# Optimization experiments

Hardware: AMD Instinct MI355X
Metric: run time of the kernel (lower is better)

Reference implementation:

```python
import jax, jax.numpy as jnp
import numpy as np

LOG2PI = float(np.log(2.0 * np.pi))
EPS_SHIFT = -0.5   # self.eps
TAU = 0.5          # self.tau
ETA = 1.0          # self.eta
MAG_A = 5500.0     # magnitude remap constants from forward()
MAG_B = 1100.0


def setup_inputs() -> dict:
    key = jax.random.key(0)
    k1, k2, k3, k4, k5 = jax.random.split(key, 5)
    B, K, C = 4096, 128, 64
    z = jax.random.normal(k1, (B, K, 2), dtype=jnp.float32)
    # per-keypoint mixture weights summing to 1 (GMM weights_)
    weights = jax.nn.softmax(jax.random.normal(k2, (K, C), dtype=jnp.float32), axis=-1)
    means = jax.random.normal(k3, (K, C, 2), dtype=jnp.float32)
    # SPD covariances: A A^T + 0.2 I
    A = jax.random.normal(k4, (K, C, 2, 2), dtype=jnp.float32) * 0.3
    covs = jnp.einsum('kcij,kclj->kcil', A, A) + 0.2 * jnp.eye(2, dtype=jnp.float32)
    # latent_stats unnormalization factor per latent coordinate (2/(max-min))
    scale = jax.random.uniform(k5, (K, 2), dtype=jnp.float32, minval=0.5, maxval=2.0)
    return {"z": z, "weights": weights, "means": means, "covs": covs, "scale": scale}


def _gmm_pdf_and_grad(z, weights, means, covs):
    # z: [B,K,2]  weights: [K,C]  means: [K,C,2]  covs: [K,C,2,2]
    a = covs[..., 0, 0]; b = covs[..., 0, 1]
    c = covs[..., 1, 0]; d = covs[..., 1, 1]
    det = a * d - b * c                                  # [K,C]
    inv00 = d / det; inv01 = -b / det
    inv10 = -c / det; inv11 = a / det
    diff = z[:, :, None, :] - means[None]                # [B,K,C,2]
    d0 = diff[..., 0]; d1 = diff[..., 1]
    s0 = inv00 * d0 + inv01 * d1                         # Sigma^{-1} diff, [B,K,C]
    s1 = inv10 * d0 + inv11 * d1
    maha = d0 * s0 + d1 * s1                             # [B,K,C]
    logp = -0.5 * (maha + jnp.log(det) + 2.0 * LOG2PI)   # MVN log_prob (D=2)
    comp = weights[None] * jnp.exp(logp)                 # weighted component densities
    pdf = comp.sum(-1)                                   # [B,K]
    # analytic grad of pdf wrt z: sum_c comp_c * (-Sigma_c^{-1} (z-mu_c))
    g0 = -(comp * s0).sum(-1)
    g1 = -(comp * s1).sum(-1)
    grad = jnp.stack([g0, g1], axis=-1)                  # [B,K,2]
    return pdf, grad


def reference(z, weights, means, covs, scale):
    B, K, _ = z.shape
    pdf, grad = _gmm_pdf_and_grad(z, weights, means, covs)
    # densities duplicated per coordinate: [pdf_i, pdf_i] per keypoint -> [B, 2K]
    densities = jnp.repeat(pdf, 2, axis=-1)
    density_norm = jax.nn.sigmoid((densities + EPS_SHIFT) / TAU)
    # unnormalize_gradient: elementwise rescale into raw latent space
    grad_raw = grad * scale[None]                        # [B,K,2]
    nrm = jnp.linalg.norm(grad_raw, axis=-1, keepdims=True)  # [B,K,1]
    mag = jnp.exp((-nrm + MAG_A) / MAG_B)
    negexp_grad = (grad_raw / nrm) * mag                 # [B,K,2]
    return density_norm, ETA * negexp_grad.reshape(B, 2 * K)
```

## Files before the change

kernel.cpp:

```cpp
#include <hip/hip_runtime.h>

#define K_KP   128
#define C_COMP 64
#define TK     16
#define TBW    16
#define NB     2
#define LDS_STRIDE 516

#if __has_builtin(__builtin_amdgcn_exp2f)
#define EXP2F(x) __builtin_amdgcn_exp2f(x)
#else
#define EXP2F(x) exp2f(x)
#endif
#if __has_builtin(__builtin_amdgcn_logf)
#define LOG2F_(x) __builtin_amdgcn_logf(x)
#else
#define LOG2F_(x) __log2f(x)
#endif
#if __has_builtin(__builtin_amdgcn_rcpf)
#define RCPF(x) __builtin_amdgcn_rcpf(x)
#else
#define RCPF(x) (1.0f/(x))
#endif
#if __has_builtin(__builtin_amdgcn_rsqf)
#define RSQF(x) __builtin_amdgcn_rsqf(x)
#else
#define RSQF(x) rsqrtf(x)
#endif

__global__ __launch_bounds__(256, 4) void recovery_kernel(
    const float* __restrict__ z,
    const float* __restrict__ weights,
    const float* __restrict__ means,
    const float* __restrict__ covs,
    const float* __restrict__ scale,
    float* __restrict__ out, int B)
{
    __shared__ float lds[TK * LDS_STRIDE];

    const int t  = threadIdx.x;
    const int kb = blockIdx.x & 7;
    const int bb = blockIdx.x >> 3;
    const int k0 = kb * TK;
    const int b0 = bb * (TBW * NB);

    const float K2       = 0.72134752044f;
    const float LOG2_2PI = 2.6514961295f;
    for (int i = t; i < TK * C_COMP; i += 256) {
        int kl = i >> 6;
        int c  = i & 63;
        int g  = (k0 + kl) * C_COMP + c;
        float w  = weights[g];
        float m0 = means[2*g], m1 = means[2*g + 1];
        float a  = covs[4*g],     bq = covs[4*g + 1];
        float cq = covs[4*g + 2], d  = covs[4*g + 3];
        float det  = a*d - bq*cq;
        float rdet = RCPF(det);
        float i00 = d  * rdet * K2;
        float i01 = -bq * rdet * K2;
        float i11 = a  * rdet * K2;
        float lc = LOG2F_(w) - LOG2_2PI - 0.5f * LOG2F_(det);
        float* p = &lds[kl * LDS_STRIDE + c * 8];
        ((float4*)p)[0] = make_float4(m0, m1, i00, i01);
        ((float2*)(p + 4))[0] = make_float2(i11, lc);
    }
    __syncthreads();

    const int kl = t & 15;
    const int bl = t >> 4;
    const int kg = k0 + kl;

    const float2* z2 = (const float2*)z;
    float zx[NB], zy[NB];
#pragma unroll
    for (int j = 0; j < NB; ++j) {
        int b = b0 + bl + j * TBW;
        float2 v = z2[(size_t)b * K_KP + kg];
        zx[j] = v.x; zy[j] = v.y;
    }

    float pdf[NB], gs0[NB], gs1[NB];
#pragma unroll
    for (int j = 0; j < NB; ++j) { pdf[j] = 0.0f; gs0[j] = 0.0f; gs1[j] = 0.0f; }

    const float* kp = &lds[kl * LDS_STRIDE];
#pragma unroll 4
    for (int c = 0; c < C_COMP; ++c) {
        float4 A  = *(const float4*)(kp + c * 8);
        float2 Bv = *(const float2*)(kp + c * 8 + 4);
        float m0 = A.x, m1 = A.y, i00 = A.z, i01 = A.w;
        float i11 = Bv.x, lc = Bv.y;
#pragma unroll
        for (int j = 0; j < NB; ++j) {
            float d0 = zx[j] - m0;
            float d1 = zy[j] - m1;
            float s0 = fmaf(i01, d1, i00 * d0);
            float s1 = fmaf(i01, d0, i11 * d1);
            float arg = fmaf(-d1, s1, lc);
            arg = fmaf(-d0, s0, arg);
            float e = EXP2F(arg);
            pdf[j] += e;
            gs0[j] = fmaf(e, s0, gs0[j]);
            gs1[j] = fmaf(e, s1, gs1[j]);
        }
    }

    float2 sc = ((const float2*)scale)[kg];
    const float NEG_INV_K2 = -1.3862943611f;
    float f0 = sc.x * NEG_INV_K2;
    float f1 = sc.y * NEG_INV_K2;
    const int KK2 = 2 * K_KP;
    float* out0 = out;
    float* out1 = out + (size_t)B * KK2;
#pragma unroll
    for (int j = 0; j < NB; ++j) {
        int b = b0 + bl + j * TBW;
        float x  = 2.0f * pdf[j] - 1.0f;
        float ex = EXP2F(-1.44269504f * x);
        float dn = RCPF(1.0f + ex);
        float g0 = gs0[j] * f0;
        float g1 = gs1[j] * f1;
        float n2 = fmaf(g0, g0, g1 * g1);
        float rn = RSQF(n2);
        float nrm = n2 * rn;
        float mag = EXP2F(fmaf(nrm, -0.0013115409f, 7.2134752044f));
        float m = rn * mag;
        ((float2*)(out0 + (size_t)b * KK2 + 2 * kg))[0] = make_float2(dn, dn);
        ((float2*)(out1 + (size_t)b * KK2 + 2 * kg))[0] = make_float2(g0 * m, g1 * m);
    }
}

extern "C" void kernel_launch(void* const* d_in, const int* in_sizes, int n_in,
                              void* d_out, int out_size, void* d_ws, size_t ws_size,
                              hipStream_t stream) {
    const float* z       = (const float*)d_in[0];
    const float* weights = (const float*)d_in[1];
    const float* means   = (const float*)d_in[2];
    const float* covs    = (const float*)d_in[3];
    const float* scale   = (const float*)d_in[4];
    float* out = (float*)d_out;

    int B = in_sizes[0] / (2 * K_KP);
    int grid = (K_KP / TK) * (B / (TBW * NB));
    recovery_kernel<<<grid, 256, 0, stream>>>(z, weights, means, covs, scale, out, B);
}
```

Measured before the change: 76.21 us.

## Vectorize GMM evaluation with packed float2 math and retile to 4 batch rows per thread

Switches the per-component Mahalanobis/exponent arithmetic to 2-wide vector types so the compiler can emit packed FP32 instructions (v_pk_fma/v_pk_mul), and processes four batch rows per thread instead of two. The tile changes to 8 keypoints by 128 batch rows, and the LDS layout is repacked so two components share one 48-byte record read with three float4 loads. This aims to cut VALU instruction count and LDS loads per evaluated component. The cost is more live registers and a grid with twice as many keypoint tiles but a quarter as many batch tiles.

Result: faster. 73.26 us (-3.9%).

```diff
diff --git a/kernel.cpp b/kernel.cpp
--- a/kernel.cpp
+++ b/kernel.cpp
@@ -2,10 +2,12 @@
 
 #define K_KP   128
 #define C_COMP 64
-#define TK     16
-#define TBW    16
-#define NB     2
-#define LDS_STRIDE 516
+#define TK     8
+#define TBS    32
+#define NB     4
+#define LDS_STRIDE 388
+
+typedef float v2f __attribute__((ext_vector_type(2)));
 
 #if __has_builtin(__builtin_amdgcn_exp2f)
 #define EXP2F(x) __builtin_amdgcn_exp2f(x)
@@ -28,6 +30,21 @@
 #define RSQF(x) rsqrtf(x)
 #endif
 
+#define EVAL(m0, m1, i00, i01, i11, lc, ZX, ZY, PDF, G0, G1)            \
+    {                                                                   \
+        v2f d0 = ZX - (m0);                                             \
+        v2f d1 = ZY - (m1);                                             \
+        v2f s0 = (i00) * d0 + (i01) * d1;   \
+        v2f s1 = (i01) * d0 + (i11) * d1;                               \
+        v2f arg = (lc) - d0 * s0 - d1 * s1;           \
+        v2f e;                                                          \
+        e.x = EXP2F(arg.x);                                             \
+        e.y = EXP2F(arg.y);                                             \
+        PDF += e;                                                       \
+        G0 += e * s0;                                                   \
+        G1 += e * s1;                                                   \
+    }
+
 __global__ __launch_bounds__(256, 4) void recovery_kernel(
     const float* __restrict__ z,
     const float* __restrict__ weights,
@@ -39,10 +56,10 @@
     __shared__ float lds[TK * LDS_STRIDE];
 
     const int t  = threadIdx.x;
-    const int kb = blockIdx.x & 7;
-    const int bb = blockIdx.x >> 3;
+    const int kb = blockIdx.x & 15;
+    const int bb = blockIdx.x >> 4;
     const int k0 = kb * TK;
-    const int b0 = bb * (TBW * NB);
+    const int b0 = bb * (TBS * NB);
 
     const float K2       = 0.72134752044f;
     const float LOG2_2PI = 2.6514961295f;
@@ -60,50 +77,46 @@
         float i01 = -bq * rdet * K2;
         float i11 = a  * rdet * K2;
         float lc = LOG2F_(w) - LOG2_2PI - 0.5f * LOG2F_(det);
-        float* p = &lds[kl * LDS_STRIDE + c * 8];
-        ((float4*)p)[0] = make_float4(m0, m1, i00, i01);
-        ((float2*)(p + 4))[0] = make_float2(i11, lc);
+        float* row = &lds[kl * LDS_STRIDE + (c >> 1) * 12];
+        ((float4*)(row + (c & 1) * 4))[0] = make_float4(m0, m1, i00, i01);
+        ((float2*)(row + 8 + (c & 1) * 2))[0] = make_float2(i11, lc);
     }
     __syncthreads();
 
-    const int kl = t & 15;
-    const int bl = t >> 4;
+    const int kl = t & 7;
+    const int bl = t >> 3;
     const int kg = k0 + kl;
 
     const float2* z2 = (const float2*)z;
     float zx[NB], zy[NB];
 #pragma unroll
     for (int j = 0; j < NB; ++j) {
-        int b = b0 + bl + j * TBW;
+        int b = b0 + bl + j * TBS;
         float2 v = z2[(size_t)b * K_KP + kg];
         zx[j] = v.x; zy[j] = v.y;
     }
 
-    float pdf[NB], gs0[NB], gs1[NB];
-#pragma unroll
-    for (int j = 0; j < NB; ++j) { pdf[j] = 0.0f; gs0[j] = 0.0f; gs1[j] = 0.0f; }
+    v2f ZXa = {zx[0], zx[1]}, ZXb = {zx[2], zx[3]};
+    v2f ZYa = {zy[0], zy[1]}, ZYb = {zy[2], zy[3]};
+    v2f pdfa = {0.f, 0.f}, pdfb = {0.f, 0.f};
+    v2f g0a  = {0.f, 0.f}, g0b  = {0.f, 0.f};
+    v2f g1a  = {0.f, 0.f}, g1b  = {0.f, 0.f};
 
     const float* kp = &lds[kl * LDS_STRIDE];
 #pragma unroll 4
-    for (int c = 0; c < C_COMP; ++c) {
-        float4 A  = *(const float4*)(kp + c * 8);
-        float2 Bv = *(const float2*)(kp + c * 8 + 4);
-        float m0 = A.x, m1 = A.y, i00 = A.z, i01 = A.w;
-        float i11 = Bv.x, lc = Bv.y;
-#pragma unroll
-        for (int j = 0; j < NB; ++j) {
-            float d0 = zx[j] - m0;
-            float d1 = zy[j] - m1;
-            float s0 = fmaf(i01, d1, i00 * d0);
-            float s1 = fmaf(i01, d0, i11 * d1);
-            float arg = fmaf(-d1, s1, lc);
-            arg = fmaf(-d0, s0, arg);
-            float e = EXP2F(arg);
-            pdf[j] += e;
-            gs0[j] = fmaf(e, s0, gs0[j]);
-            gs1[j] = fmaf(e, s1, gs1[j]);
-        }
+    for (int p = 0; p < C_COMP / 2; ++p) {
+        float4 A0 = *(const float4*)(kp + p * 12);
+        float4 A1 = *(const float4*)(kp + p * 12 + 4);
+        float4 Bp = *(const float4*)(kp + p * 12 + 8);
+        EVAL(A0.x, A0.y, A0.z, A0.w, Bp.x, Bp.y, ZXa, ZYa, pdfa, g0a, g1a);
+        EVAL(A0.x, A0.y, A0.z, A0.w, Bp.x, Bp.y, ZXb, ZYb, pdfb, g0b, g1b);
+        EVAL(A1.x, A1.y, A1.z, A1.w, Bp.z, Bp.w, ZXa, ZYa, pdfa, g0a, g1a);
+        EVAL(A1.x, A1.y, A1.z, A1.w, Bp.z, Bp.w, ZXb, ZYb, pdfb, g0b, g1b);
     }
+
+    float pdf[NB] = {pdfa.x, pdfa.y, pdfb.x, pdfb.y};
+    float gs0[NB] = {g0a.x, g0a.y, g0b.x, g0b.y};
+    float gs1[NB] = {g1a.x, g1a.y, g1b.x, g1b.y};
 
     float2 sc = ((const float2*)scale)[kg];
     const float NEG_INV_K2 = -1.3862943611f;
@@ -114,7 +127,7 @@
     float* out1 = out + (size_t)B * KK2;
 #pragma unroll
     for (int j = 0; j < NB; ++j) {
-        int b = b0 + bl + j * TBW;
+        int b = b0 + bl + j * TBS;
         float x  = 2.0f * pdf[j] - 1.0f;
         float ex = EXP2F(-1.44269504f * x);
         float dn = RCPF(1.0f + ex);
@@ -141,6 +154,6 @@
     float* out = (float*)d_out;
 
     int B = in_sizes[0] / (2 * K_KP);
-    int grid = (K_KP / TK) * (B / (TBW * NB));
+    int grid = (K_KP / TK) * (B / (TBS * NB));
     recovery_kernel<<<grid, 256, 0, stream>>>(z, weights, means, covs, scale, out, B);
 }
```
